# Optimization experiments

Hardware: AMD Instinct MI355X
Metric: run time of the kernel (lower is better)

Reference implementation:

```python
import jax, jax.numpy as jnp
import numpy as np

B, T, C, H, W_SP = 16, 256, 1024, 8, 8
OUT = 1024
ALPHA_INIT = 0.9


def setup_inputs() -> dict:
    key = jax.random.key(0)
    k_x, k_w = jax.random.split(key, 2)
    x = jax.random.normal(k_x, (B, T, C, H, W_SP), dtype=jnp.float32)
    r0 = jnp.zeros((B, OUT), dtype=jnp.float32)
    W = jax.random.normal(k_w, (OUT, C), dtype=jnp.float32) * 0.02
    b = jnp.zeros((OUT,), dtype=jnp.float32)
    alpha = jnp.full((OUT,), ALPHA_INIT, dtype=jnp.float32)
    return {"x": x, "r0": r0, "W": W, "b": b, "alpha": alpha}


def reference(x, r0, W, b, alpha):
    # x: [B, T, C, H, W] -> spatial mean -> [B, T, C]
    xm = x.mean(axis=(3, 4))
    # per-timestep linear done as one batched matmul: [B, T, OUT]
    u = jnp.einsum('btc,oc->bto', xm, W) + b
    # linear diagonal recurrence r_t = alpha * r_{t-1} + u_t
    def step(r, u_t):
        r = alpha * r + u_t
        return r, r
    r_final, r_seq = jax.lax.scan(step, r0, jnp.swapaxes(u, 0, 1))  # scan over T
    r_seq = jnp.swapaxes(r_seq, 0, 1)  # [B, T, OUT]
    return (r_seq, r_final)
```

## Files before the change

kernel.cpp:

```cpp
#include <hip/hip_runtime.h>
#include <hip/hip_bf16.h>
#include <stdint.h>


typedef __attribute__((ext_vector_type(8))) short bf16x8;
typedef __attribute__((ext_vector_type(4))) float f32x4;

__device__ __forceinline__ unsigned short f2bf(float f) {
  union { float f; unsigned int u; } c; c.f = f;
  unsigned int u = c.u;
  return (unsigned short)((u + 0x7FFFu + ((u >> 16) & 1u)) >> 16);
}

__global__ __launch_bounds__(256) void k_wcvt(const float* __restrict__ W,
                                              unsigned short* __restrict__ Wb) {
  int i = (blockIdx.x * 256 + threadIdx.x) * 4;
  float4 v = *(const float4*)(W + i);
  ushort4 o;
  o.x = f2bf(v.x); o.y = f2bf(v.y); o.z = f2bf(v.z); o.w = f2bf(v.w);
  *(ushort4*)(Wb + i) = o;
}

__global__ __launch_bounds__(256) void k_mean(const float* __restrict__ x,
                                              unsigned short* __restrict__ xm) {
  const int tid = threadIdx.x;
  const int sub = tid & 15;
  const int grp = tid >> 4;
  for (int base = blockIdx.x * 16; base < (1 << 22); base += gridDim.x * 16) {
    int seg = base + grp;
    const float4 v = *(const float4*)(x + (long)seg * 64 + sub * 4);
    float s = v.x + v.y + v.z + v.w;
    s += __shfl_xor(s, 1);
    s += __shfl_xor(s, 2);
    s += __shfl_xor(s, 4);
    s += __shfl_xor(s, 8);
    if (sub == 0) xm[seg] = f2bf(s * 0.015625f);
  }
}

#define GLDS16(g, l) \
  __builtin_amdgcn_global_load_lds((const __attribute__((address_space(1))) void*)(g), \
                                   (__attribute__((address_space(3))) void*)(l), 16, 0, 0)

__global__ __launch_bounds__(256) void k_gemm(const unsigned short* __restrict__ A,
                                              const unsigned short* __restrict__ Bm,
                                              float* __restrict__ U) {
  __shared__ unsigned short As[64 * 32];
  __shared__ unsigned short Bs[64 * 32];
  const int tid  = threadIdx.x;
  const int lane = tid & 63;
  const int wid  = tid >> 6;
  const int wr = wid >> 1, wc = wid & 1;
  const int m0 = blockIdx.y * 64, n0 = blockIdx.x * 64;

  f32x4 acc[2][2] = {};

  const int srow  = tid >> 2;
  const int sslot = tid & 3;
  const int gk0   = (sslot ^ (srow & 3)) << 3;
  const int r16   = lane & 15;
  const int kb    = lane >> 4;

  const unsigned short* ag = A  + (long)(m0 + srow) * 1024 + gk0;
  const unsigned short* bg = Bm + (long)(n0 + srow) * 1024 + gk0;

  for (int k0 = 0; k0 < 1024; k0 += 32) {
    GLDS16(ag + k0, (char*)As + tid * 16);
    GLDS16(bg + k0, (char*)Bs + tid * 16);
    __syncthreads();

    bf16x8 af[2], bfr[2];
#pragma unroll
    for (int i = 0; i < 2; i++) {
      const int rr = wr * 32 + i * 16 + r16;
      af[i] = *(const bf16x8*)(As + rr * 32 + ((kb ^ (rr & 3)) << 3));
    }
#pragma unroll
    for (int j = 0; j < 2; j++) {
      const int cc = wc * 32 + j * 16 + r16;
      bfr[j] = *(const bf16x8*)(Bs + cc * 32 + ((kb ^ (cc & 3)) << 3));
    }
#pragma unroll
    for (int i = 0; i < 2; i++)
#pragma unroll
      for (int j = 0; j < 2; j++)
        acc[i][j] = __builtin_amdgcn_mfma_f32_16x16x32_bf16(af[i], bfr[j], acc[i][j], 0, 0, 0);
    __syncthreads();
  }

  const int orow = (lane >> 4) * 4;
  const int ocol = lane & 15;
#pragma unroll
  for (int i = 0; i < 2; i++)
#pragma unroll
    for (int j = 0; j < 2; j++) {
      const int m = m0 + wr * 32 + i * 16 + orow;
      const int n = n0 + wc * 32 + j * 16 + ocol;
#pragma unroll
      for (int q = 0; q < 4; q++)
        U[(long)(m + q) * 1024 + n] = acc[i][j][q];
    }
}

__global__ __launch_bounds__(256) void k_scan(const float* __restrict__ r0,
                                              const float* __restrict__ bias,
                                              const float* __restrict__ alpha,
                                              float* __restrict__ out) {
  const int gid = blockIdx.x * 256 + threadIdx.x;
  const int o = gid & 1023;
  const float a  = alpha[o];
  const float bb = bias[o];
  float r = r0[gid];
  float* p = out + (long)(gid >> 10) * (256L * 1024) + o;
#pragma unroll 1
  for (int g = 0; g < 4; g++) {
    float buf[64];
#pragma unroll
    for (int i = 0; i < 64; i++) buf[i] = p[i * 1024];
#pragma unroll
    for (int i = 0; i < 64; i++) { r = fmaf(a, r, buf[i] + bb); buf[i] = r; }
#pragma unroll
    for (int i = 0; i < 64; i++) p[i * 1024] = buf[i];
    p += 64 * 1024;
  }
  out[(1 << 22) + gid] = r;
}

extern "C" void kernel_launch(void* const* d_in, const int* in_sizes, int n_in,
                              void* d_out, int out_size, void* d_ws, size_t ws_size,
                              hipStream_t stream) {
  const float* x     = (const float*)d_in[0];
  const float* r0    = (const float*)d_in[1];
  const float* W     = (const float*)d_in[2];
  const float* b     = (const float*)d_in[3];
  const float* alpha = (const float*)d_in[4];
  float* out = (float*)d_out;

  unsigned short* xm = (unsigned short*)d_ws;
  unsigned short* Wb = (unsigned short*)((char*)d_ws + (8u << 20));

  k_wcvt<<<1024, 256, 0, stream>>>(W, Wb);
  k_mean<<<2048, 256, 0, stream>>>(x, xm);
  dim3 g(16, 64);
  k_gemm<<<g, 256, 0, stream>>>(xm, Wb, out);
  k_scan<<<64, 256, 0, stream>>>(r0, b, alpha, out);
}
```

Baseline: 237.8 us.

## Fuse W conversion into mean, enlarge GEMM M-tile, move bias, double-buffer scan

The weight-to-bf16 conversion now runs inside the mean kernel, saving a launch. The GEMM tile grows to 128 rows per block with a revised LDS swizzle and adds the bias in its epilogue. The scan kernel now uses 64-thread blocks across 256 blocks, so more CUs take part, and double-buffers its register chunks so the next loads overlap the current recurrence. The two 64-element register buffers raise register pressure, and the larger GEMM tile halves the number of GEMM blocks.

```diff
diff --git a/kernel.cpp b/kernel.cpp
--- a/kernel.cpp
+++ b/kernel.cpp
@@ -12,18 +12,18 @@
   return (unsigned short)((u + 0x7FFFu + ((u >> 16) & 1u)) >> 16);
 }
 
-__global__ __launch_bounds__(256) void k_wcvt(const float* __restrict__ W,
+__global__ __launch_bounds__(256) void k_mean(const float* __restrict__ x,
+                                              unsigned short* __restrict__ xm,
+                                              const float* __restrict__ W,
                                               unsigned short* __restrict__ Wb) {
-  int i = (blockIdx.x * 256 + threadIdx.x) * 4;
-  float4 v = *(const float4*)(W + i);
-  ushort4 o;
-  o.x = f2bf(v.x); o.y = f2bf(v.y); o.z = f2bf(v.z); o.w = f2bf(v.w);
-  *(ushort4*)(Wb + i) = o;
-}
-
-__global__ __launch_bounds__(256) void k_mean(const float* __restrict__ x,
-                                              unsigned short* __restrict__ xm) {
   const int tid = threadIdx.x;
+  const int wi = blockIdx.x * 256 + tid;
+  if (wi < 262144) {
+    float4 v = *(const float4*)(W + wi * 4);
+    ushort4 o;
+    o.x = f2bf(v.x); o.y = f2bf(v.y); o.z = f2bf(v.z); o.w = f2bf(v.w);
+    *(ushort4*)(Wb + wi * 4) = o;
+  }
   const int sub = tid & 15;
   const int grp = tid >> 4;
   for (int base = blockIdx.x * 16; base < (1 << 22); base += gridDim.x * 16) {
@@ -42,46 +42,50 @@
   __builtin_amdgcn_global_load_lds((const __attribute__((address_space(1))) void*)(g), \
                                    (__attribute__((address_space(3))) void*)(l), 16, 0, 0)
 
+__device__ __forceinline__ int swz(int r) { return (r & 3) ^ ((r >> 2) & 3); }
+
 __global__ __launch_bounds__(256) void k_gemm(const unsigned short* __restrict__ A,
                                               const unsigned short* __restrict__ Bm,
+                                              const float* __restrict__ bias,
                                               float* __restrict__ U) {
-  __shared__ unsigned short As[64 * 32];
+  __shared__ unsigned short As[128 * 32];
   __shared__ unsigned short Bs[64 * 32];
   const int tid  = threadIdx.x;
   const int lane = tid & 63;
   const int wid  = tid >> 6;
   const int wr = wid >> 1, wc = wid & 1;
-  const int m0 = blockIdx.y * 64, n0 = blockIdx.x * 64;
+  const int m0 = blockIdx.y * 128, n0 = blockIdx.x * 64;
 
-  f32x4 acc[2][2] = {};
+  f32x4 acc[4][2] = {};
 
   const int srow  = tid >> 2;
   const int sslot = tid & 3;
-  const int gk0   = (sslot ^ (srow & 3)) << 3;
   const int r16   = lane & 15;
   const int kb    = lane >> 4;
 
-  const unsigned short* ag = A  + (long)(m0 + srow) * 1024 + gk0;
-  const unsigned short* bg = Bm + (long)(n0 + srow) * 1024 + gk0;
+  const unsigned short* ag0 = A  + (long)(m0 + srow) * 1024 + ((sslot ^ swz(srow)) << 3);
+  const unsigned short* ag1 = A  + (long)(m0 + 64 + srow) * 1024 + ((sslot ^ swz(srow + 64)) << 3);
+  const unsigned short* bg  = Bm + (long)(n0 + srow) * 1024 + ((sslot ^ swz(srow)) << 3);
 
   for (int k0 = 0; k0 < 1024; k0 += 32) {
-    GLDS16(ag + k0, (char*)As + tid * 16);
-    GLDS16(bg + k0, (char*)Bs + tid * 16);
+    GLDS16(ag0 + k0, (char*)As + tid * 16);
+    GLDS16(ag1 + k0, (char*)As + tid * 16 + 4096);
+    GLDS16(bg  + k0, (char*)Bs + tid * 16);
     __syncthreads();
 
-    bf16x8 af[2], bfr[2];
+    bf16x8 af[4], bfr[2];
 #pragma unroll
-    for (int i = 0; i < 2; i++) {
-      const int rr = wr * 32 + i * 16 + r16;
-      af[i] = *(const bf16x8*)(As + rr * 32 + ((kb ^ (rr & 3)) << 3));
+    for (int i = 0; i < 4; i++) {
+      const int rr = wr * 64 + i * 16 + r16;
+      af[i] = *(const bf16x8*)(As + rr * 32 + ((kb ^ swz(rr)) << 3));
     }
 #pragma unroll
     for (int j = 0; j < 2; j++) {
       const int cc = wc * 32 + j * 16 + r16;
-      bfr[j] = *(const bf16x8*)(Bs + cc * 32 + ((kb ^ (cc & 3)) << 3));
+      bfr[j] = *(const bf16x8*)(Bs + cc * 32 + ((kb ^ swz(cc)) << 3));
     }
 #pragma unroll
-    for (int i = 0; i < 2; i++)
+    for (int i = 0; i < 4; i++)
 #pragma unroll
       for (int j = 0; j < 2; j++)
         acc[i][j] = __builtin_amdgcn_mfma_f32_16x16x32_bf16(af[i], bfr[j], acc[i][j], 0, 0, 0);
@@ -90,39 +94,46 @@
 
   const int orow = (lane >> 4) * 4;
   const int ocol = lane & 15;
+  const float bb[2] = { bias[n0 + wc * 32 + ocol], bias[n0 + wc * 32 + 16 + ocol] };
 #pragma unroll
-  for (int i = 0; i < 2; i++)
+  for (int i = 0; i < 4; i++)
 #pragma unroll
     for (int j = 0; j < 2; j++) {
-      const int m = m0 + wr * 32 + i * 16 + orow;
+      const int m = m0 + wr * 64 + i * 16 + orow;
       const int n = n0 + wc * 32 + j * 16 + ocol;
 #pragma unroll
       for (int q = 0; q < 4; q++)
-        U[(long)(m + q) * 1024 + n] = acc[i][j][q];
+        U[(long)(m + q) * 1024 + n] = acc[i][j][q] + bb[j];
     }
 }
 
-__global__ __launch_bounds__(256) void k_scan(const float* __restrict__ r0,
-                                              const float* __restrict__ bias,
-                                              const float* __restrict__ alpha,
-                                              float* __restrict__ out) {
-  const int gid = blockIdx.x * 256 + threadIdx.x;
+template<int G>
+__device__ __forceinline__ void scan_load(float* buf, const float* p) {
+#pragma unroll
+  for (int i = 0; i < 64; i++) buf[i] = p[G * 65536 + i * 1024];
+}
+template<int G>
+__device__ __forceinline__ void scan_proc(float* buf, float* p, float a, float& r) {
+#pragma unroll
+  for (int i = 0; i < 64; i++) { r = fmaf(a, r, buf[i]); buf[i] = r; }
+#pragma unroll
+  for (int i = 0; i < 64; i++) p[G * 65536 + i * 1024] = buf[i];
+}
+
+__global__ __launch_bounds__(64) void k_scan(const float* __restrict__ r0,
+                                             const float* __restrict__ alpha,
+                                             float* __restrict__ out) {
+  const int gid = blockIdx.x * 64 + threadIdx.x;
   const int o = gid & 1023;
-  const float a  = alpha[o];
-  const float bb = bias[o];
+  const float a = alpha[o];
   float r = r0[gid];
   float* p = out + (long)(gid >> 10) * (256L * 1024) + o;
-#pragma unroll 1
-  for (int g = 0; g < 4; g++) {
-    float buf[64];
-#pragma unroll
-    for (int i = 0; i < 64; i++) buf[i] = p[i * 1024];
-#pragma unroll
-    for (int i = 0; i < 64; i++) { r = fmaf(a, r, buf[i] + bb); buf[i] = r; }
-#pragma unroll
-    for (int i = 0; i < 64; i++) p[i * 1024] = buf[i];
-    p += 64 * 1024;
-  }
+  float bufA[64], bufB[64];
+  scan_load<0>(bufA, p);
+  scan_load<1>(bufB, p); scan_proc<0>(bufA, p, a, r);
+  scan_load<2>(bufA, p); scan_proc<1>(bufB, p, a, r);
+  scan_load<3>(bufB, p); scan_proc<2>(bufA, p, a, r);
+  scan_proc<3>(bufB, p, a, r);
   out[(1 << 22) + gid] = r;
 }
 
@@ -139,9 +150,8 @@
   unsigned short* xm = (unsigned short*)d_ws;
   unsigned short* Wb = (unsigned short*)((char*)d_ws + (8u << 20));
 
-  k_wcvt<<<1024, 256, 0, stream>>>(W, Wb);
-  k_mean<<<2048, 256, 0, stream>>>(x, xm);
-  dim3 g(16, 64);
-  k_gemm<<<g, 256, 0, stream>>>(xm, Wb, out);
-  k_scan<<<64, 256, 0, stream>>>(r0, b, alpha, out);
+  k_mean<<<2048, 256, 0, stream>>>(x, xm, W, Wb);
+  dim3 g(16, 32);
+  k_gemm<<<g, 256, 0, stream>>>(xm, Wb, b, out);
+  k_scan<<<256, 64, 0, stream>>>(r0, alpha, out);
 }
```

Result: no change. 235.5 us (-0.9%).
